# Kernel optimization log

Measured on AMD Instinct MI355X. Metric: run time of the kernel, lower is better.

Reference implementation:

```python
import jax, jax.numpy as jnp
import numpy as np

N = 2048        # samples per batch
IN = 256        # in_size
OUT = 256       # out_size
T = 128         # num_tasks


def setup_inputs() -> dict:
    key = jax.random.key(0)
    k1, k2, k3 = jax.random.split(key, 3)
    inputs = jax.random.normal(k1, (N, IN), dtype=jnp.float32)
    task_ids = jax.random.randint(k2, (N,), 0, T, dtype=jnp.int64)
    # Task-specific weight table [num_tasks, in_size, out_size],
    # kaiming-style scale 1/sqrt(in_size).
    W = jax.random.normal(k3, (T, IN, OUT), dtype=jnp.float32) / jnp.sqrt(
        jnp.float32(IN)
    )
    return {"inputs": inputs, "task_ids": task_ids, "W": W}


def reference(inputs, task_ids, W):
    # _get_matrices: gather per-sample weight matrix by task id -> [N, in, out]
    mats = W[task_ids]
    # einsum 'ni,nio->no': per-sample matvec
    return jnp.einsum("ni,nio->no", inputs, mats)
```

## Files before the change

kernel.cpp:

```cpp
#include <hip/hip_runtime.h>
#include <hip/hip_bf16.h>


#define NSAMP 2048
#define NTASK 128
#define INSZ  256
#define OUTSZ 256
#define CHUNK 8
#define NDESC 384
#define NBLK2 (NDESC * 2)


__global__ __launch_bounds__(256, 1)
void k1_build(const int* __restrict__ ids32, int* __restrict__ ws)
{
    __shared__ int cnt[NTASK];
    __shared__ int cur[NTASK];
    __shared__ int cbase[NTASK];
    __shared__ int chbase[NTASK];
    __shared__ int scanbuf[256];
    __shared__ int s_odd, s_total;

    const int tid = threadIdx.x;
    if (tid == 0) s_odd = 0;
    if (tid < NTASK) cnt[tid] = 0;
    __syncthreads();

    int any = 0;
    for (int j = 1 + 2 * tid; j < NSAMP; j += 512) any |= ids32[j];
    if (any) s_odd = 1;
    __syncthreads();
    const bool is64 = (s_odd == 0);

    int myid[8];
    #pragma unroll
    for (int j = 0; j < 8; ++j) {
        int n = tid * 8 + j;
        myid[j] = is64 ? ids32[2 * n] : ids32[n];
        atomicAdd(&cnt[myid[j]], 1);
    }
    __syncthreads();

    {
        int t = tid & 127;
        scanbuf[tid] = (tid < 128) ? cnt[t] : ((cnt[t] + CHUNK - 1) >> 3);
        __syncthreads();
        #pragma unroll
        for (int off = 1; off < 128; off <<= 1) {
            int v = scanbuf[tid];
            if (t >= off) v += scanbuf[tid - off];
            __syncthreads();
            scanbuf[tid] = v;
            __syncthreads();
        }
        if (tid < 128) {
            cbase[tid] = scanbuf[tid] - cnt[tid];
            cur[tid]   = scanbuf[tid] - cnt[tid];
        } else {
            chbase[t] = scanbuf[tid] - ((cnt[t] + CHUNK - 1) >> 3);
            if (tid == 255) s_total = scanbuf[255];
        }
    }
    __syncthreads();

    #pragma unroll
    for (int j = 0; j < 8; ++j) {
        int n = tid * 8 + j;
        int pos = atomicAdd(&cur[myid[j]], 1);
        ws[pos] = n;
    }

    if (tid < NTASK) {
        const int c  = cnt[tid];
        const int cb = cbase[tid];
        int slot = NSAMP + chbase[tid];
        for (int c0 = 0; c0 < c; c0 += CHUNK) {
            int len = min(CHUNK, c - c0);
            ws[slot++] = tid | (len << 8) | ((cb + c0) << 16);
        }
    }
    const int total = s_total;
    for (int i = total + tid; i < NDESC; i += 256)
        ws[NSAMP + i] = 0;
}

__global__ __launch_bounds__(256, 2)
void k2_gemv(const float* __restrict__ X, const float* __restrict__ W,
             const int* __restrict__ ws, float* __restrict__ out)
{
    __shared__ float xt[INSZ * CHUNK];
    __shared__ float pacc[4 * CHUNK * 128];
    __shared__ int   s_n[CHUNK];

    const int bx = blockIdx.x;
    const int dlin = (bx & 7) * (NBLK2 / 8) + (bx >> 3);
    const int slot = dlin >> 1;
    const int half = dlin & 1;
    const int desc = ws[NSAMP + slot];
    const int len  = (desc >> 8) & 0xff;
    if (len == 0) return;
    const int task  = desc & 0xff;
    const int start = desc >> 16;

    const int tid  = threadIdx.x;
    const int lane = tid & 63;
    const int wv   = tid >> 6;

    if (tid < CHUNK) s_n[tid] = (tid < len) ? ws[start + tid] : -1;

    #pragma unroll
    for (int s = 0; s < CHUNK; ++s) {
        float v = 0.f;
        if (s < len) { int n = ws[start + s]; v = X[(size_t)n * INSZ + tid]; }
        xt[tid * CHUNK + s] = v;
    }
    __syncthreads();

    const int col0 = half * 128 + lane * 2;
    const float* wp = W + ((size_t)task * INSZ + wv * 64) * OUTSZ + col0;

    float2 acc[CHUNK];
    #pragma unroll
    for (int s = 0; s < CHUNK; ++s) acc[s] = make_float2(0.f, 0.f);

    #pragma unroll 8
    for (int i = 0; i < 64; ++i) {
        const float2 w2 = *(const float2*)wp;
        const float4 xa = *(const float4*)&xt[(wv * 64 + i) * CHUNK];
        const float4 xb = *(const float4*)&xt[(wv * 64 + i) * CHUNK + 4];
        acc[0].x += xa.x * w2.x; acc[0].y += xa.x * w2.y;
        acc[1].x += xa.y * w2.x; acc[1].y += xa.y * w2.y;
        acc[2].x += xa.z * w2.x; acc[2].y += xa.z * w2.y;
        acc[3].x += xa.w * w2.x; acc[3].y += xa.w * w2.y;
        acc[4].x += xb.x * w2.x; acc[4].y += xb.x * w2.y;
        acc[5].x += xb.y * w2.x; acc[5].y += xb.y * w2.y;
        acc[6].x += xb.z * w2.x; acc[6].y += xb.z * w2.y;
        acc[7].x += xb.w * w2.x; acc[7].y += xb.w * w2.y;
        wp += OUTSZ;
    }

    float* pb = &pacc[wv * (CHUNK * 128) + lane * 2];
    #pragma unroll
    for (int s = 0; s < CHUNK; ++s)
        *(float2*)&pb[s * 128] = acc[s];
    __syncthreads();

    {
        const int e = tid * 4;
        float4 v = make_float4(0.f, 0.f, 0.f, 0.f);
        #pragma unroll
        for (int w2i = 0; w2i < 4; ++w2i) {
            const float4 p = *(const float4*)&pacc[w2i * 1024 + e];
            v.x += p.x; v.y += p.y; v.z += p.z; v.w += p.w;
        }
        const int s  = e >> 7;
        const int lc = e & 127;
        const int n  = s_n[s];
        if (n >= 0)
            *(float4*)&out[(size_t)n * OUTSZ + half * 128 + lc] = v;
    }
}

extern "C" void kernel_launch(void* const* d_in, const int* in_sizes, int n_in,
                              void* d_out, int out_size, void* d_ws, size_t ws_size,
                              hipStream_t stream) {
    const float* X   = (const float*)d_in[0];
    const int*   ids = (const int*)d_in[1];
    const float* W   = (const float*)d_in[2];
    float*       out = (float*)d_out;
    int*         wsi = (int*)d_ws;

    k1_build<<<1, 256, 0, stream>>>(ids, wsi);
    k2_gemv<<<NBLK2, 256, 0, stream>>>(X, W, wsi, out);
}
```

Before: 89.54 us.

## Pack two chunk jobs per 512-thread block with register-prefetched weight rows

The grid changes from 768 blocks of 256 threads (one chunk-half each) to 256 blocks of 512 threads. Each half-block handles one full chunk job, looping over both output halves, and job count comes from a total stored by the build kernel. Weight rows are loaded into a double-buffered register prefetch of 8 rows to hide global latency. The aim is to reuse the gathered X tile across both output halves and cut launch and empty-block overhead. The cost is more registers and serialised halves per block, which gives less parallelism per job.

```diff
diff --git a/kernel.cpp b/kernel.cpp
--- a/kernel.cpp
+++ b/kernel.cpp
@@ -8,7 +8,7 @@
 #define OUTSZ 256
 #define CHUNK 8
 #define NDESC 384
-#define NBLK2 (NDESC * 2)
+#define PF    8
 
 
 __global__ __launch_bounds__(256, 1)
@@ -82,82 +82,115 @@
     const int total = s_total;
     for (int i = total + tid; i < NDESC; i += 256)
         ws[NSAMP + i] = 0;
+    if (tid == 0) ws[NSAMP + NDESC] = total;
 }
 
-__global__ __launch_bounds__(256, 2)
+__global__ __launch_bounds__(512, 2)
 void k2_gemv(const float* __restrict__ X, const float* __restrict__ W,
              const int* __restrict__ ws, float* __restrict__ out)
 {
-    __shared__ float xt[INSZ * CHUNK];
-    __shared__ float pacc[4 * CHUNK * 128];
-    __shared__ int   s_n[CHUNK];
-
-    const int bx = blockIdx.x;
-    const int dlin = (bx & 7) * (NBLK2 / 8) + (bx >> 3);
-    const int slot = dlin >> 1;
-    const int half = dlin & 1;
-    const int desc = ws[NSAMP + slot];
-    const int len  = (desc >> 8) & 0xff;
-    if (len == 0) return;
-    const int task  = desc & 0xff;
-    const int start = desc >> 16;
+    __shared__ float xt[2][INSZ * CHUNK];
+    __shared__ float pacc[2][4 * CHUNK * 128];
+    __shared__ int   s_n[2][CHUNK];
 
     const int tid  = threadIdx.x;
-    const int lane = tid & 63;
-    const int wv   = tid >> 6;
-
-    if (tid < CHUNK) s_n[tid] = (tid < len) ? ws[start + tid] : -1;
+    const int hb   = tid >> 8;
+    const int ht   = tid & 255;
+    const int lane = ht & 63;
+    const int wl   = ht >> 6;
+
+    const int total = ws[NSAMP + NDESC];
+    const int job   = blockIdx.x + hb * 256;
+
+    int task = 0, start = 0, len = 0;
+    if (job < total) {
+        const int desc = ws[NSAMP + job];
+        task  = desc & 0xff;
+        len   = (desc >> 8) & 0xff;
+        start = desc >> 16;
+    }
+    const bool active = (len > 0);
+
+    if (ht < CHUNK) s_n[hb][ht] = (ht < len) ? ws[start + ht] : -1;
+    __syncthreads();
 
     #pragma unroll
     for (int s = 0; s < CHUNK; ++s) {
+        const int n = s_n[hb][s];
         float v = 0.f;
-        if (s < len) { int n = ws[start + s]; v = X[(size_t)n * INSZ + tid]; }
-        xt[tid * CHUNK + s] = v;
-    }
-    __syncthreads();
-
-    const int col0 = half * 128 + lane * 2;
-    const float* wp = W + ((size_t)task * INSZ + wv * 64) * OUTSZ + col0;
-
-    float2 acc[CHUNK];
-    #pragma unroll
-    for (int s = 0; s < CHUNK; ++s) acc[s] = make_float2(0.f, 0.f);
-
-    #pragma unroll 8
-    for (int i = 0; i < 64; ++i) {
-        const float2 w2 = *(const float2*)wp;
-        const float4 xa = *(const float4*)&xt[(wv * 64 + i) * CHUNK];
-        const float4 xb = *(const float4*)&xt[(wv * 64 + i) * CHUNK + 4];
-        acc[0].x += xa.x * w2.x; acc[0].y += xa.x * w2.y;
-        acc[1].x += xa.y * w2.x; acc[1].y += xa.y * w2.y;
-        acc[2].x += xa.z * w2.x; acc[2].y += xa.z * w2.y;
-        acc[3].x += xa.w * w2.x; acc[3].y += xa.w * w2.y;
-        acc[4].x += xb.x * w2.x; acc[4].y += xb.x * w2.y;
-        acc[5].x += xb.y * w2.x; acc[5].y += xb.y * w2.y;
-        acc[6].x += xb.z * w2.x; acc[6].y += xb.z * w2.y;
-        acc[7].x += xb.w * w2.x; acc[7].y += xb.w * w2.y;
-        wp += OUTSZ;
-    }
-
-    float* pb = &pacc[wv * (CHUNK * 128) + lane * 2];
-    #pragma unroll
-    for (int s = 0; s < CHUNK; ++s)
-        *(float2*)&pb[s * 128] = acc[s];
-    __syncthreads();
-
-    {
-        const int e = tid * 4;
-        float4 v = make_float4(0.f, 0.f, 0.f, 0.f);
+        if (n >= 0) v = X[(size_t)n * INSZ + ht];
+        xt[hb][ht * CHUNK + s] = v;
+    }
+    __syncthreads();
+
+    for (int half = 0; half < 2; ++half) {
+        float2 acc[CHUNK];
         #pragma unroll
-        for (int w2i = 0; w2i < 4; ++w2i) {
-            const float4 p = *(const float4*)&pacc[w2i * 1024 + e];
-            v.x += p.x; v.y += p.y; v.z += p.z; v.w += p.w;
-        }
-        const int s  = e >> 7;
-        const int lc = e & 127;
-        const int n  = s_n[s];
-        if (n >= 0)
-            *(float4*)&out[(size_t)n * OUTSZ + half * 128 + lc] = v;
+        for (int s = 0; s < CHUNK; ++s) acc[s] = make_float2(0.f, 0.f);
+
+        if (active) {
+            const int col0 = half * 128 + lane * 2;
+            const float* wp = W + ((size_t)task * INSZ + wl * 64) * OUTSZ + col0;
+
+            float2 wbuf[PF];
+            #pragma unroll
+            for (int k = 0; k < PF; ++k)
+                wbuf[k] = *(const float2*)(wp + k * OUTSZ);
+
+            #pragma unroll
+            for (int g = 0; g < 64 / PF; ++g) {
+                float2 wnext[PF];
+                if (g < 64 / PF - 1) {
+                    #pragma unroll
+                    for (int k = 0; k < PF; ++k)
+                        wnext[k] = *(const float2*)(wp + ((g + 1) * PF + k) * OUTSZ);
+                }
+                #pragma unroll
+                for (int k = 0; k < PF; ++k) {
+                    const int i = g * PF + k;
+                    const float2 w2 = wbuf[k];
+                    const float4 xa = *(const float4*)&xt[hb][(wl * 64 + i) * CHUNK];
+                    const float4 xb = *(const float4*)&xt[hb][(wl * 64 + i) * CHUNK + 4];
+                    acc[0].x += xa.x * w2.x; acc[0].y += xa.x * w2.y;
+                    acc[1].x += xa.y * w2.x; acc[1].y += xa.y * w2.y;
+                    acc[2].x += xa.z * w2.x; acc[2].y += xa.z * w2.y;
+                    acc[3].x += xa.w * w2.x; acc[3].y += xa.w * w2.y;
+                    acc[4].x += xb.x * w2.x; acc[4].y += xb.x * w2.y;
+                    acc[5].x += xb.y * w2.x; acc[5].y += xb.y * w2.y;
+                    acc[6].x += xb.z * w2.x; acc[6].y += xb.z * w2.y;
+                    acc[7].x += xb.w * w2.x; acc[7].y += xb.w * w2.y;
+                }
+                if (g < 64 / PF - 1) {
+                    #pragma unroll
+                    for (int k = 0; k < PF; ++k)
+                        wbuf[k] = wnext[k];
+                }
+            }
+        }
+
+        {
+            float* pb = &pacc[hb][wl * (CHUNK * 128) + lane * 2];
+            #pragma unroll
+            for (int s = 0; s < CHUNK; ++s)
+                *(float2*)&pb[s * 128] = acc[s];
+        }
+        __syncthreads();
+
+        {
+            const int e = ht * 4;
+            float4 v = make_float4(0.f, 0.f, 0.f, 0.f);
+            #pragma unroll
+            for (int q = 0; q < 4; ++q) {
+                const float4 p = *(const float4*)&pacc[hb][q * 1024 + e];
+                v.x += p.x; v.y += p.y; v.z += p.z; v.w += p.w;
+            }
+            const int s  = e >> 7;
+            const int lc = e & 127;
+            const int n  = s_n[hb][s];
+            if (n >= 0)
+                *(float4*)&out[(size_t)n * OUTSZ + half * 128 + lc] = v;
+        }
+        __syncthreads();
     }
 }
 
@@ -171,5 +204,5 @@
     int*         wsi = (int*)d_ws;
 
     k1_build<<<1, 256, 0, stream>>>(ids, wsi);
-    k2_gemv<<<NBLK2, 256, 0, stream>>>(X, W, wsi, out);
+    k2_gemv<<<256, 512, 0, stream>>>(X, W, wsi, out);
 }
```

After: 94.73 us. +5.8%, slower.
